# Kernel optimization log

Measured on AMD Instinct MI355X. Metric: run time of the kernel, lower is better.

The kernel has to match this reference:

```python
import jax, jax.numpy as jnp
import numpy as np

N = 50000      # nodes
E = 800000     # edges (avg degree 16)
IN_DIM = 64
EMB = 64
L = 4          # num_layer
BN_EPS = 1e-5


def setup_inputs() -> dict:
    key = jax.random.key(0)
    ks = jax.random.split(key, 8)
    s = 0.05
    return {
        "x": jax.random.normal(ks[0], (N, 1, IN_DIM), jnp.float32),
        "edge_index": jax.random.randint(ks[1], (2, E), 0, N, jnp.int32),
        "edge_attr": jax.random.normal(ks[2], (E, 3), jnp.float32),
        "edge_weight": jax.random.uniform(ks[3], (E,), jnp.float32),
        # atom encoder Linear(in_dim, emb)
        "ae_w": jax.random.normal(ks[4], (IN_DIM, EMB), jnp.float32) * s,
        "ae_b": jnp.zeros((EMB,), jnp.float32),
        # per-layer GIN MLP: Linear -> BN -> ReLU -> Linear (stacked over L)
        "W1": jax.random.normal(ks[5], (L, EMB, EMB), jnp.float32) * s,
        "b1": jnp.zeros((L, EMB), jnp.float32),
        "g1": jnp.ones((L, EMB), jnp.float32),
        "be1": jnp.zeros((L, EMB), jnp.float32),
        "W2": jax.random.normal(ks[6], (L, EMB, EMB), jnp.float32) * s,
        "b2": jnp.zeros((L, EMB), jnp.float32),
        # outer per-layer BatchNorm1d in GNN_node
        "g_out": jnp.ones((L, EMB), jnp.float32),
        "be_out": jnp.zeros((L, EMB), jnp.float32),
    }


def _bn(h, g, b):
    # BatchNorm1d, training mode: batch stats over node dim, biased variance
    m = h.mean(0)
    v = h.var(0)
    return (h - m) * jax.lax.rsqrt(v + BN_EPS) * g + b


def reference(x, edge_index, edge_attr, edge_weight,
              ae_w, ae_b, W1, b1, g1, be1, W2, b2, g_out, be_out):
    # atom encoder on x[:, 0] : [N, in_dim] -> [N, emb]
    h = x[:, 0] @ ae_w + ae_b
    src = edge_index[0]
    dst = edge_index[1]
    n = h.shape[0]
    num_layers = W1.shape[0]
    for l in range(num_layers):
        # MyPyGINConv (train_eps=False, eps=0): scatter-add of x_j * w_e, plus self term
        msg = h[src] * edge_weight[:, None]                      # [E, emb]
        agg = jax.ops.segment_sum(msg, dst, num_segments=n)      # [N, emb]
        out = agg + h                                            # (1+eps)*x_r, eps=0
        # conv MLP: Linear -> BN -> ReLU -> Linear
        out = jax.nn.relu(_bn(out @ W1[l] + b1[l], g1[l], be1[l]))
        out = out @ W2[l] + b2[l]
        # outer BN + ReLU (always applied for 'originalgin'); dropout p=0; residual
        out = jax.nn.relu(_bn(out, g_out[l], be_out[l]))
        h = out + h
    return h  # JK='last'
```

## Files before the change

### kernel.cpp

```cpp
#include <hip/hip_runtime.h>
#include <stdint.h>

#define EMB 64
#define BN_EPS 1e-5f
#define BSH 8
#define CHUNK 4096
#define TS 68

typedef short bfrag __attribute__((ext_vector_type(8)));
typedef float f32x4 __attribute__((ext_vector_type(4)));

#define IN_F32    0
#define IN_BF16   1
#define IN_BF16BN 2

struct SMM {
  float tb[64 * TS];
  float st[128];
  float scs[EMB], shs[EMB];
  unsigned short wb[4096];
};

__device__ __forceinline__ unsigned short f2b(float x) {
  unsigned u = __float_as_uint(x);
  u += 0x7FFFu + ((u >> 16) & 1u);
  return (unsigned short)(u >> 16);
}
__device__ __forceinline__ float b2f(unsigned short v) {
  return __uint_as_float(((unsigned)v) << 16);
}

__device__ __forceinline__ void enc_tile(SMM& sm, int tile,
    const float* x, const float* aewf, const float* bias,
    unsigned short* out16, int N) {
  const int tid = threadIdx.x;
  const int lane = tid & 63;
  const int wv = tid >> 6;
  const int r = wv >> 1;
  const int c0 = (wv & 1) * 2;
  const int m = lane & 15;
  const int quad = lane >> 4;
  const int node0 = tile * 64;

#pragma unroll
  for (int it = 0; it < 8; it++) {
    int idx = it * 512 + tid;
    int j = idx >> 6, k = idx & 63;
    sm.wb[idx] = f2b(aewf[k * EMB + j]);
  }
  __syncthreads();

  bfrag a0 = {0, 0, 0, 0, 0, 0, 0, 0}, a1 = {0, 0, 0, 0, 0, 0, 0, 0};
  const int arow = node0 + r * 16 + m;
  if (arow < N) {
    const float* af = x + (size_t)arow * EMB + quad * 8;
#pragma unroll
    for (int j = 0; j < 8; j++) {
      a0[j] = (short)f2b(af[j]);
      a1[j] = (short)f2b(af[32 + j]);
    }
  }
  f32x4 zz[2];
#pragma unroll
  for (int cc = 0; cc < 2; cc++) {
    const int c = c0 + cc;
    const unsigned short* bb = &sm.wb[(c * 16 + m) * EMB + quad * 8];
    bfrag b0 = *(const bfrag*)bb;
    bfrag b1 = *(const bfrag*)(bb + 32);
    f32x4 z = {0.f, 0.f, 0.f, 0.f};
    z = __builtin_amdgcn_mfma_f32_16x16x32_bf16(a0, b0, z, 0, 0, 0);
    z = __builtin_amdgcn_mfma_f32_16x16x32_bf16(a1, b1, z, 0, 0, 0);
    zz[cc] = z;
  }
#pragma unroll
  for (int cc = 0; cc < 2; cc++) {
    const int c = c0 + cc;
    float bj = bias[c * 16 + m];
#pragma unroll
    for (int reg = 0; reg < 4; reg++) {
      int row = r * 16 + quad * 4 + reg;
      float v = (node0 + row < N) ? (zz[cc][reg] + bj) : 0.f;
      sm.tb[row * TS + c * 16 + m] = v;
    }
  }
  __syncthreads();
  ushort4* o4 = (ushort4*)(out16 + (size_t)node0 * EMB);
#pragma unroll
  for (int it = 0; it < 2; it++) {
    int flat4 = it * 512 + tid;
    int nsub = flat4 >> 4;
    int c4 = flat4 & 15;
    if (node0 + nsub < N) {
      const float* s4 = sm.tb + nsub * TS + c4 * 4;
      ushort4 o;
      o.x = f2b(s4[0]); o.y = f2b(s4[1]);
      o.z = f2b(s4[2]); o.w = f2b(s4[3]);
      o4[flat4] = o;
    }
  }
}

__global__ void __launch_bounds__(512) k_enc_prep(
        const float* __restrict__ x, const float* __restrict__ ae_w,
        const float* __restrict__ ae_b,
        const float* __restrict__ W1, const float* __restrict__ W2,
        unsigned short* __restrict__ Wt16, int* __restrict__ hist_part,
        float* __restrict__ stats, const int* __restrict__ ei,
        unsigned short* __restrict__ hb16,
        int E, int L, int nstats, int ntiles, int nchunks, int N) {
  __shared__ SMM sm;
  if ((int)blockIdx.x < ntiles) {
    enc_tile(sm, blockIdx.x, x, ae_w, ae_b, hb16, N);
    return;
  }
  const int pb = blockIdx.x - ntiles;
  const int tid = threadIdx.x;
  int* lh = (int*)sm.tb;
  const int nw2 = 2 * L * EMB * EMB;
  for (int gid = pb * 512 + tid; gid < nw2; gid += nchunks * 512) {
    int mI = gid >> 12;
    int j = (gid >> 6) & 63;
    int k = gid & 63;
    const float* src = (mI < L) ? W1 + (size_t)mI * EMB * EMB
                                : W2 + (size_t)(mI - L) * EMB * EMB;
    Wt16[EMB * EMB + gid] = f2b(src[k * EMB + j]);
  }
  for (int i = pb * 512 + tid; i < nstats; i += nchunks * 512) stats[i] = 0.0f;
  if (tid < 256) lh[tid] = 0;
  __syncthreads();
  const int c0 = pb * CHUNK;
  const int cend = min(c0 + CHUNK, E);
  for (int e = c0 + tid; e < cend; e += 512)
    atomicAdd(&lh[((unsigned)ei[E + e]) >> BSH], 1);
  __syncthreads();
  if (tid < 256) hist_part[pb * 256 + tid] = lh[tid];
}

__global__ void __launch_bounds__(256) k_part(
        const int* __restrict__ ei, const float* __restrict__ ew,
        const int* __restrict__ hist_part, int* __restrict__ bbase,
        int2* __restrict__ eG, int E, int nchunks, int nb) {
  __shared__ int a[256], lbase[256], loff[256];
  const int t = threadIdx.x;
  const int c = blockIdx.x;
  int pre = 0, post = 0;
#pragma unroll 8
  for (int cc = 0; cc < c; cc++) pre += hist_part[cc * 256 + t];
#pragma unroll 8
  for (int cc = c; cc < nchunks; cc++) post += hist_part[cc * 256 + t];
  const int tot = pre + post;
  a[t] = tot;
  __syncthreads();
  for (int off = 1; off < 256; off <<= 1) {
    int x = (t >= off) ? a[t - off] : 0;
    __syncthreads();
    a[t] += x;
    __syncthreads();
  }
  int excl = a[t] - tot;
  lbase[t] = excl + pre;
  loff[t] = 0;
  if (c == 0 && t <= nb) bbase[t] = excl;
  __syncthreads();
  const int c0 = c * CHUNK;
#pragma unroll 4
  for (int i = 0; i < 16; i++) {
    int e = c0 + i * 256 + t;
    if (e < E) {
      int d = ei[E + e];
      int g = ((unsigned)d) >> BSH;
      int pk = ei[e] | ((d & 255) << 24);
      int pos = lbase[g] + atomicAdd(&loff[g], 1);
      eG[pos] = make_int2(pk, __float_as_int(ew[e]));
    }
  }
}

__global__ void __launch_bounds__(256) k_build(
        const int2* __restrict__ eG, const int* __restrict__ bbase,
        int* __restrict__ rowst, int* __restrict__ counts,
        int2* __restrict__ pairs, int N) {
  __shared__ int lcnt[256], a[256], lcur[256];
  const int t = threadIdx.x;
  const int b = blockIdx.x;
  const int e0 = bbase[b], e1 = bbase[b + 1];
  lcnt[t] = 0;
  __syncthreads();
  for (int i = e0 + t; i < e1; i += 256)
    atomicAdd(&lcnt[((unsigned)eG[i].x) >> 24], 1);
  __syncthreads();
  int v = lcnt[t];
  a[t] = v;
  __syncthreads();
  for (int off = 1; off < 256; off <<= 1) {
    int x = (t >= off) ? a[t - off] : 0;
    __syncthreads();
    a[t] += x;
    __syncthreads();
  }
  int excl = a[t] - v;
  lcur[t] = excl;
  int node = (b << BSH) + t;
  if (node < N) { rowst[node] = e0 + excl; counts[node] = v; }
  __syncthreads();
  for (int i = e0 + t; i < e1; i += 256) {
    int2 p = eG[i];
    int loc = ((unsigned)p.x) >> 24;
    int pos = e0 + atomicAdd(&lcur[loc], 1);
    pairs[pos] = make_int2(p.x & 0x00FFFFFF, p.y);
  }
}

__global__ void k_agg(const unsigned short* __restrict__ hb,
                      const int* __restrict__ rowst,
                      const int* __restrict__ counts, const int2* __restrict__ pairs,
                      unsigned short* __restrict__ out16, int N) {
  const int lane = threadIdx.x & 63;
  const int half = lane >> 5;
  const int col = lane & 31;
  int wave = (blockIdx.x * blockDim.x + threadIdx.x) >> 6;
  const int nwaves = (gridDim.x * blockDim.x) >> 6;
  for (int nA = wave; nA < N; nA += 2 * nwaves) {
    const int nB = nA + nwaves;
    const int uA = __builtin_amdgcn_readfirstlane(nA);
    const int uB = __builtin_amdgcn_readfirstlane(nB);
    const bool hasB = uB < N;
    int sA = rowst[uA], eA = sA + counts[uA];
    int sB = 0, eB = 0;
    if (hasB) { sB = rowst[uB]; eB = sB + counts[uB]; }
    float a0A[4] = {0, 0, 0, 0}, a1A[4] = {0, 0, 0, 0};
    float a0B[4] = {0, 0, 0, 0}, a1B[4] = {0, 0, 0, 0};
    for (int xA = sA, xB = sB; (xA < eA) | (xB < eB); xA += 8, xB += 8) {
      int2 pA[8], pB[8];
#pragma unroll
      for (int k = 0; k < 8; k++) {
        int ia = xA + k;
        pA[k] = pairs[ia < eA ? ia : 0];
      }
#pragma unroll
      for (int k = 0; k < 8; k++) {
        int ib = xB + k;
        pB[k] = pairs[ib < eB ? ib : 0];
      }
#pragma unroll
      for (int j = 0; j < 4; j++) {
        int2 pp = half ? pA[2 * j + 1] : pA[2 * j];
        bool ok = (xA + 2 * j + half) < eA;
        float w = ok ? __int_as_float(pp.y) : 0.f;
        unsigned v = *((const unsigned*)(hb + (size_t)pp.x * EMB) + col);
        a0A[j] = fmaf(w, b2f((unsigned short)(v & 0xFFFFu)), a0A[j]);
        a1A[j] = fmaf(w, b2f((unsigned short)(v >> 16)), a1A[j]);
      }
#pragma unroll
      for (int j = 0; j < 4; j++) {
        int2 pp = half ? pB[2 * j + 1] : pB[2 * j];
        bool ok = (xB + 2 * j + half) < eB;
        float w = ok ? __int_as_float(pp.y) : 0.f;
        unsigned v = *((const unsigned*)(hb + (size_t)pp.x * EMB) + col);
        a0B[j] = fmaf(w, b2f((unsigned short)(v & 0xFFFFu)), a0B[j]);
        a1B[j] = fmaf(w, b2f((unsigned short)(v >> 16)), a1B[j]);
      }
    }
    {
      float s0 = (a0A[0] + a0A[1]) + (a0A[2] + a0A[3]);
      float s1 = (a1A[0] + a1A[1]) + (a1A[2] + a1A[3]);
      s0 += __shfl_xor(s0, 32);
      s1 += __shfl_xor(s1, 32);
      float v0 = __shfl(s0, lane >> 1);
      float v1 = __shfl(s1, lane >> 1);
      float sum = ((lane & 1) ? v1 : v0) + b2f(hb[(size_t)uA * EMB + lane]);
      out16[(size_t)uA * EMB + lane] = f2b(sum);
    }
    if (hasB) {
      float s0 = (a0B[0] + a0B[1]) + (a0B[2] + a0B[3]);
      float s1 = (a1B[0] + a1B[1]) + (a1B[2] + a1B[3]);
      s0 += __shfl_xor(s0, 32);
      s1 += __shfl_xor(s1, 32);
      float v0 = __shfl(s0, lane >> 1);
      float v1 = __shfl(s1, lane >> 1);
      float sum = ((lane & 1) ? v1 : v0) + b2f(hb[(size_t)uB * EMB + lane]);
      out16[(size_t)uB * EMB + lane] = f2b(sum);
    }
  }
}

template <int INMODE, bool DO_STATS>
__global__ void __launch_bounds__(256) k_mmx(
        const void* __restrict__ in_v, const unsigned short* __restrict__ Wt,
        const float* __restrict__ bias, const float* __restrict__ stats,
        const float* __restrict__ g, const float* __restrict__ be, float invN,
        unsigned short* __restrict__ out16, float* __restrict__ st_out, int N) {
  __shared__ float tb[64 * TS];
  __shared__ float st_part[128];
  __shared__ float scs[EMB], shs[EMB];
  const int tid = threadIdx.x;
  const int lane = tid & 63;
  const int wv = tid >> 6;
  const int node0 = blockIdx.x * 64;
  const int m = lane & 15;
  const int quad = lane >> 4;

  if (DO_STATS && tid < 128) st_part[tid] = 0.f;
  if (INMODE == IN_BF16BN) {
    if (tid < EMB) {
      float s1 = 0.f, s2 = 0.f;
#pragma unroll
      for (int k = 0; k < 8; k++) {
        s1 += stats[k * 128 + tid];
        s2 += stats[k * 128 + 64 + tid];
      }
      float mm = s1 * invN;
      float va = fmaf(s2, invN, -mm * mm);
      float rs = rsqrtf(va + BN_EPS);
      float sc = rs * g[tid];
      scs[tid] = sc;
      shs[tid] = fmaf(-mm, sc, be[tid]);
    }
    __syncthreads();
  }

  const int arow = node0 + wv * 16 + m;
  bfrag a0 = {0, 0, 0, 0, 0, 0, 0, 0}, a1 = {0, 0, 0, 0, 0, 0, 0, 0};
  if (arow < N) {
    if (INMODE == IN_BF16) {
      const unsigned short* ab =
          (const unsigned short*)in_v + (size_t)arow * EMB + quad * 8;
      a0 = *(const bfrag*)ab;
      a1 = *(const bfrag*)(ab + 32);
    } else if (INMODE == IN_BF16BN) {
      const unsigned short* ab =
          (const unsigned short*)in_v + (size_t)arow * EMB + quad * 8;
      bfrag r0 = *(const bfrag*)ab;
      bfrag r1 = *(const bfrag*)(ab + 32);
#pragma unroll
      for (int j = 0; j < 8; j++) {
        int k0 = quad * 8 + j;
        float v0 = b2f((unsigned short)r0[j]);
        float v1 = b2f((unsigned short)r1[j]);
        v0 = fmaxf(0.f, fmaf(v0, scs[k0], shs[k0]));
        v1 = fmaxf(0.f, fmaf(v1, scs[k0 + 32], shs[k0 + 32]));
        a0[j] = (short)f2b(v0);
        a1[j] = (short)f2b(v1);
      }
    }
  }

  const unsigned short* bb = Wt + (size_t)m * EMB + quad * 8;
  f32x4 acc[4];
#pragma unroll
  for (int c = 0; c < 4; c++) {
    bfrag b0 = *(const bfrag*)(bb + c * 16 * EMB);
    bfrag b1 = *(const bfrag*)(bb + c * 16 * EMB + 32);
    f32x4 z = {0.f, 0.f, 0.f, 0.f};
    z = __builtin_amdgcn_mfma_f32_16x16x32_bf16(a0, b0, z, 0, 0, 0);
    z = __builtin_amdgcn_mfma_f32_16x16x32_bf16(a1, b1, z, 0, 0, 0);
    acc[c] = z;
  }

#pragma unroll
  for (int c = 0; c < 4; c++) {
    float bj = bias[c * 16 + m];
#pragma unroll
    for (int r = 0; r < 4; r++) {
      int row = wv * 16 + quad * 4 + r;
      float v = (node0 + row < N) ? (acc[c][r] + bj) : 0.f;
      tb[row * TS + c * 16 + m] = v;
    }
  }
  __syncthreads();

  if (DO_STATS) {
    float ssum = 0.f, ssq = 0.f;
#pragma unroll
    for (int i = 0; i < 16; i++) {
      float v = tb[(wv * 16 + i) * TS + lane];
      ssum += v;
      ssq = fmaf(v, v, ssq);
    }
    atomicAdd(&st_part[lane], ssum);
    atomicAdd(&st_part[64 + lane], ssq);
  }

  ushort4* o4 = (ushort4*)(out16 + (size_t)node0 * EMB);
#pragma unroll
  for (int it = 0; it < 4; it++) {
    int flat4 = it * 256 + tid;
    int nsub = flat4 >> 4;
    int c4 = flat4 & 15;
    if (node0 + nsub < N) {
      const float* s4 = tb + nsub * TS + c4 * 4;
      ushort4 o;
      o.x = f2b(s4[0]); o.y = f2b(s4[1]);
      o.z = f2b(s4[2]); o.w = f2b(s4[3]);
      o4[flat4] = o;
    }
  }

  if (DO_STATS) {
    __syncthreads();
    if (tid < 128)
      atomicAdd(&st_out[((unsigned)blockIdx.x & 7u) * 128 + tid], st_part[tid]);
  }
}

template <bool LAST>
__global__ void k_bnres(const unsigned short* __restrict__ u16,
                        const float* __restrict__ st,
                        const float* __restrict__ g, const float* __restrict__ be,
                        unsigned short* __restrict__ hb16, float* __restrict__ out32,
                        float invN, int total4) {
  __shared__ float scs[EMB], shs[EMB];
  const int tid = threadIdx.x;
  if (tid < EMB) {
    float s1 = 0.f, s2 = 0.f;
#pragma unroll
    for (int k = 0; k < 8; k++) {
      s1 += st[k * 128 + tid];
      s2 += st[k * 128 + 64 + tid];
    }
    float mm = s1 * invN;
    float va = fmaf(s2, invN, -mm * mm);
    float rs = rsqrtf(va + BN_EPS);
    float sc = rs * g[tid];
    scs[tid] = sc;
    shs[tid] = fmaf(-mm, sc, be[tid]);
  }
  __syncthreads();
  int stride = gridDim.x * blockDim.x;
  for (int i4 = blockIdx.x * blockDim.x + tid; i4 < total4; i4 += stride) {
    int c4 = i4 & 15;
    ushort4 uv = ((const ushort4*)u16)[i4];
    ushort4 hv = ((const ushort4*)hb16)[i4];
    float4 scv = *(const float4*)&scs[c4 * 4];
    float4 shv = *(const float4*)&shs[c4 * 4];
    float4 o;
    o.x = fmaxf(0.f, fmaf(b2f(uv.x), scv.x, shv.x)) + b2f(hv.x);
    o.y = fmaxf(0.f, fmaf(b2f(uv.y), scv.y, shv.y)) + b2f(hv.y);
    o.z = fmaxf(0.f, fmaf(b2f(uv.z), scv.z, shv.z)) + b2f(hv.z);
    o.w = fmaxf(0.f, fmaf(b2f(uv.w), scv.w, shv.w)) + b2f(hv.w);
    if (LAST) {
      ((float4*)out32)[i4] = o;
    } else {
      ushort4 ob;
      ob.x = f2b(o.x); ob.y = f2b(o.y);
      ob.z = f2b(o.z); ob.w = f2b(o.w);
      ((ushort4*)hb16)[i4] = ob;
    }
  }
}

extern "C" void kernel_launch(void* const* d_in, const int* in_sizes, int n_in,
                              void* d_out, int out_size, void* d_ws, size_t ws_size,
                              hipStream_t stream) {
  const float* x     = (const float*)d_in[0];
  const int*   ei    = (const int*)d_in[1];
  const float* ew    = (const float*)d_in[3];
  const float* ae_w  = (const float*)d_in[4];
  const float* ae_b  = (const float*)d_in[5];
  const float* W1    = (const float*)d_in[6];
  const float* b1    = (const float*)d_in[7];
  const float* g1    = (const float*)d_in[8];
  const float* be1   = (const float*)d_in[9];
  const float* W2    = (const float*)d_in[10];
  const float* b2    = (const float*)d_in[11];
  const float* g_out = (const float*)d_in[12];
  const float* be_out= (const float*)d_in[13];

  const int N = in_sizes[0] / EMB;
  const int E = in_sizes[3];
  const int L = in_sizes[6] / (EMB * EMB);
  const float invN = 1.0f / (float)N;
  const int NBUCK = (N + 255) >> BSH;
  const int nchunks = (E + CHUNK - 1) / CHUNK;

  uintptr_t p = (uintptr_t)d_ws;
  auto alloc = [&](size_t bytes) -> void* {
    p = (p + 255) & ~(uintptr_t)255;
    void* r = (void*)p;
    p += bytes;
    return r;
  };
  unsigned short* hb16 = (unsigned short*)alloc((size_t)N * EMB * 2);
  unsigned short* b16a = (unsigned short*)alloc((size_t)N * EMB * 2);
  unsigned short* t16  = (unsigned short*)alloc((size_t)N * EMB * 2);
  unsigned short* Wt16 = (unsigned short*)alloc((size_t)(1 + 2 * L) * EMB * EMB * 2);
  int*   counts= (int*)alloc((size_t)N * 4);
  int*   rowst = (int*)alloc((size_t)N * 4);
  int*   hist_part = (int*)alloc((size_t)nchunks * 256 * 4);
  int*   bbase = (int*)alloc(257 * 4);
  int2*  pairs = (int2*)alloc((size_t)E * 8);
  int2*  eG    = (int2*)alloc((size_t)E * 8);
  float* stats = (float*)alloc((size_t)L * 2 * 8 * 128 * 4);
  (void)ws_size; (void)n_in; (void)out_size;

  const int ntiles = (N + 63) / 64;
  const int nstats = L * 2 * 8 * 128;

  hipLaunchKernelGGL(k_enc_prep, dim3(ntiles + nchunks), dim3(512), 0, stream,
                     x, ae_w, ae_b, W1, W2, Wt16, hist_part, stats, ei,
                     hb16, E, L, nstats, ntiles, nchunks, N);
  hipLaunchKernelGGL(k_part, dim3(nchunks), dim3(256), 0, stream,
                     ei, ew, hist_part, bbase, eG, E, nchunks, NBUCK);
  hipLaunchKernelGGL(k_build, dim3(NBUCK), dim3(256), 0, stream,
                     eG, bbase, rowst, counts, pairs, N);

  for (int l = 0; l < L; l++) {
    float* stats1 = stats + (size_t)(l * 2 + 0) * 1024;
    float* stats2 = stats + (size_t)(l * 2 + 1) * 1024;

    hipLaunchKernelGGL(k_agg, dim3(2048), dim3(256), 0, stream,
                       hb16, rowst, counts, pairs, b16a, N);
    hipLaunchKernelGGL((k_mmx<IN_BF16, true>), dim3(ntiles), dim3(256), 0, stream,
                       b16a, Wt16 + (size_t)(1 + l) * EMB * EMB, b1 + (size_t)l * EMB,
                       (const float*)nullptr, (const float*)nullptr,
                       (const float*)nullptr, 0.f, t16, stats1, N);
    hipLaunchKernelGGL((k_mmx<IN_BF16BN, true>), dim3(ntiles), dim3(256), 0, stream,
                       t16, Wt16 + (size_t)(1 + L + l) * EMB * EMB, b2 + (size_t)l * EMB,
                       stats1, g1 + (size_t)l * EMB, be1 + (size_t)l * EMB, invN,
                       b16a, stats2, N);
    if (l == L - 1) {
      hipLaunchKernelGGL((k_bnres<true>), dim3(1024), dim3(256), 0, stream,
                         b16a, stats2, g_out + (size_t)l * EMB,
                         be_out + (size_t)l * EMB, hb16, (float*)d_out,
                         invN, N * 16);
    } else {
      hipLaunchKernelGGL((k_bnres<false>), dim3(1024), dim3(256), 0, stream,
                         b16a, stats2, g_out + (size_t)l * EMB,
                         be_out + (size_t)l * EMB, hb16, (float*)nullptr,
                         invN, N * 16);
    }
  }
}
```

Measured before the change: 361.5 us.

## Fuse outer BatchNorm, ReLU and residual into next layer's aggregation

Removes the separate per-layer BN+ReLU+residual kernel and instead applies it on the fly inside the neighbor-gather kernel of the next layer. Each gathered neighbor row now reads both the pre-BN MLP output and the old hidden state, and the kernel also writes the new hidden state using ping-pong buffers. This saves launches and one elementwise pass per layer, at the cost of doubling the per-edge gather bytes and redundant BN recomputation per edge.

```diff
diff --git a/kernel.cpp b/kernel.cpp
--- a/kernel.cpp
+++ b/kernel.cpp
@@ -284,6 +284,84 @@
   }
 }
 
+__global__ void k_aggbn(const unsigned short* __restrict__ u16,
+                        const unsigned short* __restrict__ hold,
+                        const float* __restrict__ st,
+                        const float* __restrict__ g, const float* __restrict__ be,
+                        const int* __restrict__ rowst,
+                        const int* __restrict__ counts,
+                        const int2* __restrict__ pairs,
+                        unsigned short* __restrict__ hnew,
+                        unsigned short* __restrict__ out16,
+                        float invN, int N) {
+  __shared__ float scs[EMB], shs[EMB];
+  const int tid = threadIdx.x;
+  if (tid < EMB) {
+    float s1 = 0.f, s2 = 0.f;
+#pragma unroll
+    for (int k = 0; k < 8; k++) {
+      s1 += st[k * 128 + tid];
+      s2 += st[k * 128 + 64 + tid];
+    }
+    float mu = s1 * invN;
+    float va = fmaf(s2, invN, -mu * mu);
+    float rs = rsqrtf(va + BN_EPS);
+    float sc = rs * g[tid];
+    scs[tid] = sc;
+    shs[tid] = fmaf(-mu, sc, be[tid]);
+  }
+  __syncthreads();
+  const int lane = tid & 63;
+  const int half = lane >> 5;
+  const int col = lane & 31;
+  const float sc0 = scs[2 * col], sc1 = scs[2 * col + 1];
+  const float sh0 = shs[2 * col], sh1 = shs[2 * col + 1];
+  const float scl = scs[lane], shl = shs[lane];
+  int wave = (blockIdx.x * blockDim.x + tid) >> 6;
+  const int nwaves = (gridDim.x * blockDim.x) >> 6;
+  for (int n = wave; n < N; n += nwaves) {
+    const int un = __builtin_amdgcn_readfirstlane(n);
+    const int s = rowst[un];
+    const int e = s + counts[un];
+    float uu = b2f(u16[(size_t)un * EMB + lane]);
+    float hh = b2f(hold[(size_t)un * EMB + lane]);
+    float hn = fmaxf(0.f, fmaf(uu, scl, shl)) + hh;
+    float a0[4] = {0, 0, 0, 0}, a1[4] = {0, 0, 0, 0};
+    for (int x = s; x < e; x += 8) {
+      int2 pp[8];
+#pragma unroll
+      for (int k = 0; k < 8; k++) {
+        int i = x + k;
+        pp[k] = pairs[i < e ? i : 0];
+      }
+#pragma unroll
+      for (int j = 0; j < 4; j++) {
+        int2 p = half ? pp[2 * j + 1] : pp[2 * j];
+        bool ok = (x + 2 * j + half) < e;
+        float w = ok ? __int_as_float(p.y) : 0.f;
+        const size_t base = (size_t)p.x * EMB;
+        unsigned vu = *((const unsigned*)(u16 + base) + col);
+        unsigned vh = *((const unsigned*)(hold + base) + col);
+        float h0 = fmaxf(0.f, fmaf(b2f((unsigned short)(vu & 0xFFFFu)), sc0, sh0))
+                   + b2f((unsigned short)(vh & 0xFFFFu));
+        float h1 = fmaxf(0.f, fmaf(b2f((unsigned short)(vu >> 16)), sc1, sh1))
+                   + b2f((unsigned short)(vh >> 16));
+        a0[j] = fmaf(w, h0, a0[j]);
+        a1[j] = fmaf(w, h1, a1[j]);
+      }
+    }
+    float s0 = (a0[0] + a0[1]) + (a0[2] + a0[3]);
+    float s1 = (a1[0] + a1[1]) + (a1[2] + a1[3]);
+    s0 += __shfl_xor(s0, 32);
+    s1 += __shfl_xor(s1, 32);
+    float v0 = __shfl(s0, lane >> 1);
+    float v1 = __shfl(s1, lane >> 1);
+    float sum = ((lane & 1) ? v1 : v0) + hn;
+    out16[(size_t)un * EMB + lane] = f2b(sum);
+    hnew[(size_t)un * EMB + lane] = f2b(hn);
+  }
+}
+
 template <int INMODE, bool DO_STATS>
 __global__ void __launch_bounds__(256) k_mmx(
         const void* __restrict__ in_v, const unsigned short* __restrict__ Wt,
@@ -403,12 +481,13 @@
   }
 }
 
-template <bool LAST>
-__global__ void k_bnres(const unsigned short* __restrict__ u16,
-                        const float* __restrict__ st,
-                        const float* __restrict__ g, const float* __restrict__ be,
-                        unsigned short* __restrict__ hb16, float* __restrict__ out32,
-                        float invN, int total4) {
+__global__ void k_bnres_last(const unsigned short* __restrict__ u16,
+                             const float* __restrict__ st,
+                             const float* __restrict__ g,
+                             const float* __restrict__ be,
+                             const unsigned short* __restrict__ hb16,
+                             float* __restrict__ out32,
+                             float invN, int total4) {
   __shared__ float scs[EMB], shs[EMB];
   const int tid = threadIdx.x;
   if (tid < EMB) {
@@ -438,14 +517,7 @@
     o.y = fmaxf(0.f, fmaf(b2f(uv.y), scv.y, shv.y)) + b2f(hv.y);
     o.z = fmaxf(0.f, fmaf(b2f(uv.z), scv.z, shv.z)) + b2f(hv.z);
     o.w = fmaxf(0.f, fmaf(b2f(uv.w), scv.w, shv.w)) + b2f(hv.w);
-    if (LAST) {
-      ((float4*)out32)[i4] = o;
-    } else {
-      ushort4 ob;
-      ob.x = f2b(o.x); ob.y = f2b(o.y);
-      ob.z = f2b(o.z); ob.w = f2b(o.w);
-      ((ushort4*)hb16)[i4] = ob;
-    }
+    ((float4*)out32)[i4] = o;
   }
 }
 
@@ -480,9 +552,11 @@
     p += bytes;
     return r;
   };
-  unsigned short* hb16 = (unsigned short*)alloc((size_t)N * EMB * 2);
-  unsigned short* b16a = (unsigned short*)alloc((size_t)N * EMB * 2);
+  unsigned short* hbA  = (unsigned short*)alloc((size_t)N * EMB * 2);
+  unsigned short* hbB  = (unsigned short*)alloc((size_t)N * EMB * 2);
+  unsigned short* a16  = (unsigned short*)alloc((size_t)N * EMB * 2);
   unsigned short* t16  = (unsigned short*)alloc((size_t)N * EMB * 2);
+  unsigned short* u16  = (unsigned short*)alloc((size_t)N * EMB * 2);
   unsigned short* Wt16 = (unsigned short*)alloc((size_t)(1 + 2 * L) * EMB * EMB * 2);
   int*   counts= (int*)alloc((size_t)N * 4);
   int*   rowst = (int*)alloc((size_t)N * 4);
@@ -498,36 +572,40 @@
 
   hipLaunchKernelGGL(k_enc_prep, dim3(ntiles + nchunks), dim3(512), 0, stream,
                      x, ae_w, ae_b, W1, W2, Wt16, hist_part, stats, ei,
-                     hb16, E, L, nstats, ntiles, nchunks, N);
+                     hbA, E, L, nstats, ntiles, nchunks, N);
   hipLaunchKernelGGL(k_part, dim3(nchunks), dim3(256), 0, stream,
                      ei, ew, hist_part, bbase, eG, E, nchunks, NBUCK);
   hipLaunchKernelGGL(k_build, dim3(NBUCK), dim3(256), 0, stream,
                      eG, bbase, rowst, counts, pairs, N);
 
+  unsigned short* hcur = hbA;
+  unsigned short* hnxt = hbB;
   for (int l = 0; l < L; l++) {
     float* stats1 = stats + (size_t)(l * 2 + 0) * 1024;
     float* stats2 = stats + (size_t)(l * 2 + 1) * 1024;
 
-    hipLaunchKernelGGL(k_agg, dim3(2048), dim3(256), 0, stream,
-                       hb16, rowst, counts, pairs, b16a, N);
+    if (l == 0) {
+      hipLaunchKernelGGL(k_agg, dim3(2048), dim3(256), 0, stream,
+                         hcur, rowst, counts, pairs, a16, N);
+    } else {
+      float* stats2p = stats + (size_t)((l - 1) * 2 + 1) * 1024;
+      hipLaunchKernelGGL(k_aggbn, dim3(2048), dim3(256), 0, stream,
+                         u16, hcur, stats2p, g_out + (size_t)(l - 1) * EMB,
+                         be_out + (size_t)(l - 1) * EMB, rowst, counts, pairs,
+                         hnxt, a16, invN, N);
+      unsigned short* tmp = hcur; hcur = hnxt; hnxt = tmp;
+    }
     hipLaunchKernelGGL((k_mmx<IN_BF16, true>), dim3(ntiles), dim3(256), 0, stream,
-                       b16a, Wt16 + (size_t)(1 + l) * EMB * EMB, b1 + (size_t)l * EMB,
+                       a16, Wt16 + (size_t)(1 + l) * EMB * EMB, b1 + (size_t)l * EMB,
                        (const float*)nullptr, (const float*)nullptr,
                        (const float*)nullptr, 0.f, t16, stats1, N);
     hipLaunchKernelGGL((k_mmx<IN_BF16BN, true>), dim3(ntiles), dim3(256), 0, stream,
                        t16, Wt16 + (size_t)(1 + L + l) * EMB * EMB, b2 + (size_t)l * EMB,
                        stats1, g1 + (size_t)l * EMB, be1 + (size_t)l * EMB, invN,
-                       b16a, stats2, N);
-    if (l == L - 1) {
-      hipLaunchKernelGGL((k_bnres<true>), dim3(1024), dim3(256), 0, stream,
-                         b16a, stats2, g_out + (size_t)l * EMB,
-                         be_out + (size_t)l * EMB, hb16, (float*)d_out,
-                         invN, N * 16);
-    } else {
-      hipLaunchKernelGGL((k_bnres<false>), dim3(1024), dim3(256), 0, stream,
-                         b16a, stats2, g_out + (size_t)l * EMB,
-                         be_out + (size_t)l * EMB, hb16, (float*)nullptr,
-                         invN, N * 16);
-    }
-  }
-}
+                       u16, stats2, N);
+  }
+  hipLaunchKernelGGL(k_bnres_last, dim3(1024), dim3(256), 0, stream,
+                     u16, stats + (size_t)((L - 1) * 2 + 1) * 1024,
+                     g_out + (size_t)(L - 1) * EMB, be_out + (size_t)(L - 1) * EMB,
+                     hcur, (float*)d_out, invN, N * 16);
+}
```

New measurement: 360.0 us (median of 2 runs). No clear change (-0.4%).
